# Performance work log

Hardware: AMD Instinct MI355X
Metric: run time of the kernel (lower is better)

Reference implementation:

```python
import jax, jax.numpy as jnp
import numpy as np

B, C, T = 8, 256, 2048
K = 10                     # n_neigh_seq
TEMPORAL_SCALE = 2048
SHORT_RATIO = 0.4
STITCH_GAP = 20


def setup_inputs() -> dict:
    key = jax.random.key(0)
    k1, k2, k3, k4 = jax.random.split(key, 4)
    x = jax.random.normal(k1, (B, C, T), dtype=jnp.float32)
    num_frms = jax.random.randint(k2, (B,), 0, 2048, dtype=jnp.int64 if jax.config.jax_enable_x64 else jnp.int32)
    W_conv = jax.random.normal(k3, (C, C, 3), dtype=jnp.float32) * 0.02  # Conv1d(out,in,k)
    b_conv = jnp.zeros((C,), dtype=jnp.float32)
    W_mlp = jax.random.normal(k4, (C, 2 * C), dtype=jnp.float32) * 0.02  # Linear(2C -> C)
    b_mlp = jnp.zeros((C,), dtype=jnp.float32)
    return {"x": x, "num_frms": num_frms, "W_conv": W_conv, "b_conv": b_conv,
            "W_mlp": W_mlp, "b_mlp": b_mlp}


def knn_neigh_idx(x, num_frms, k=K):
    """Vectorized translation of knn() + get_neigh_idx_semantic()."""
    b, c, t = x.shape
    ratio = TEMPORAL_SCALE / t
    half1 = k // 2
    half2 = k - half1
    # pairwise squared distances via ||xi||^2 + ||xj||^2 - 2 xi.xj (same math,
    # avoids the B*C*T*T intermediate the torch code materializes)
    sq = jnp.sum(x * x, axis=1)                           # [B,T]
    gram = jnp.einsum('bci,bcj->bij', x, x)               # [B,T,T]
    dif = sq[:, :, None] + sq[:, None, :] - 2.0 * gram    # [B,T,T]
    _, idx_org = jax.lax.top_k(-dif, k)                   # smallest-k -> [B,T,k]
    big = jnp.max(dif) + 1.0
    # per-batch short-video rewiring (original does a python loop over batch)
    cond = num_frms.astype(jnp.float32) <= SHORT_RATIO * TEMPORAL_SCALE   # [B]
    thr = (num_frms.astype(jnp.float32) + STITCH_GAP) / ratio             # [B]
    pos = jnp.arange(t)
    region = (pos[None, :, None] >= thr[:, None, None]) & \
             (pos[None, None, :] >= thr[:, None, None])                   # [B,T,T]
    dif_m = jnp.where(region, big, dif)
    # kill the already-chosen first half of neighbors, then re-topk the rest
    b_idx = jnp.arange(b)[:, None, None]
    r_idx = pos[None, :, None]
    dif_m = dif_m.at[b_idx, r_idx, idx_org[:, :, :half1]].set(big)
    _, idx2 = jax.lax.top_k(-dif_m, half2)                # [B,T,half2]
    tail = jnp.where(cond[:, None, None], idx2, idx_org[:, :, half1:])
    idx_new = jnp.concatenate([idx_org[:, :, :half1], tail], axis=-1)     # [B,T,k]
    shift = (jnp.arange(b) * t)[:, None, None]
    return (idx_new + shift).reshape(-1)                  # [B*T*k] flat node ids


def reference(x, num_frms, W_conv, b_conv, W_mlp, b_mlp):
    b, c, t = x.shape
    # tconv1: Conv1d k=3, s=1, p=1
    c_out = jax.lax.conv_general_dilated(
        x, W_conv, window_strides=(1,), padding=[(1, 1)],
        dimension_numbers=('NCH', 'OIH', 'NCH')) + b_conv[None, :, None]   # [B,C,T]
    # NeighConv on raw x (gcn_insert == 'par'), nfeat_mode='feat_ctr', agg='max'
    neigh = knn_neigh_idx(x, num_frms)                    # [B*T*K]
    feat = jnp.transpose(x, (0, 2, 1)).reshape(-1, c)     # [B*T, C]
    feat_neigh = feat[neigh].reshape(-1, K, c)            # [B*T, K, C]
    ctr = jnp.broadcast_to(feat[:, None, :], feat_neigh.shape)
    cat = jnp.concatenate([feat_neigh, ctr], axis=-1)     # [B*T, K, 2C]
    g = jnp.einsum('nkd,od->nko', cat, W_mlp) + b_mlp     # [B*T, K, C]
    g = jnp.max(g, axis=1)                                # max aggregation
    g_out = jnp.transpose(g.reshape(b, t, -1), (0, 2, 1)) # [B,C,T]
    out = jax.nn.relu(c_out + g_out)
    # MaxPool1d(kernel=2, stride=2)
    out = out.reshape(b, out.shape[1], t // 2, 2).max(axis=-1)
    return out
```

## Files before the change

### kernel.cpp

```cpp
#include <hip/hip_runtime.h>
#include <hip/hip_bf16.h>
#include <math.h>
#include <float.h>

#define NC 256
#define NT 2048

typedef __attribute__((ext_vector_type(4))) float f32x4;
typedef __attribute__((ext_vector_type(8))) short short8;
typedef __attribute__((ext_vector_type(8))) unsigned short ushort8;

#define SQ_OFF 0
#define A_OFF  131072
#define XL_OFF 8388608
#define E_OFF  16908288
#define NB_OFF 33685504

__device__ __forceinline__ int load_nf(const int* __restrict__ nf, int b) {
    bool is64 = (nf[1] == 0) & (nf[3] == 0) & (nf[5] == 0) & (nf[7] == 0);
    return is64 ? nf[2 * b] : nf[b];
}

__device__ __forceinline__ void split_bf16(float f, unsigned short& h, unsigned short& l) {
    __hip_bfloat16 hb = __float2bfloat16(f);
    float fh = __bfloat162float(hb);
    __hip_bfloat16 lb = __float2bfloat16(f - fh);
    h = *(unsigned short*)&hb;
    l = *(unsigned short*)&lb;
}

__device__ __forceinline__ float rl_f(float v, int srclane) {
    return __int_as_float(__builtin_amdgcn_readlane(__float_as_int(v), srclane));
}
__device__ __forceinline__ int rl_i(int v, int srclane) {
    return __builtin_amdgcn_readlane(v, srclane);
}
__device__ __forceinline__ float dpp_shr1_f(float v) {
    return __int_as_float(__builtin_amdgcn_update_dpp(0, __float_as_int(v), 0x111, 0xf, 0xf, false));
}
__device__ __forceinline__ int dpp_shr1_i(int v) {
    return __builtin_amdgcn_update_dpp(0, v, 0x111, 0xf, 0xf, false);
}

__global__ __launch_bounds__(256) void k_sqt(const float* __restrict__ x, double* __restrict__ sq,
                                             unsigned short* __restrict__ Xh8,
                                             unsigned short* __restrict__ Xl8,
                                             float* __restrict__ xT) {
    __shared__ double part[32][33];
    int b = blockIdx.y;
    int q0 = blockIdx.x * 32;
    int tid = threadIdx.x;
    int tq = tid & 7;
    int cg = tid >> 3;
    const float* xp = x + (size_t)b * NC * NT + q0 + tq * 4;
    double a0 = 0.0, a1 = 0.0, a2 = 0.0, a3 = 0.0;
    ushort8 hv[4], lw[4];
    float xv[4][8];
    #pragma unroll
    for (int i = 0; i < 8; ++i) {
        int c = cg * 8 + i;
        float4 f4 = *(const float4*)&xp[(size_t)c * NT];
        unsigned short h, l;
        split_bf16(f4.x, h, l); hv[0][i] = h; lw[0][i] = l; xv[0][i] = f4.x;
        a0 = fma((double)f4.x, (double)f4.x, a0);
        split_bf16(f4.y, h, l); hv[1][i] = h; lw[1][i] = l; xv[1][i] = f4.y;
        a1 = fma((double)f4.y, (double)f4.y, a1);
        split_bf16(f4.z, h, l); hv[2][i] = h; lw[2][i] = l; xv[2][i] = f4.z;
        a2 = fma((double)f4.z, (double)f4.z, a2);
        split_bf16(f4.w, h, l); hv[3][i] = h; lw[3][i] = l; xv[3][i] = f4.w;
        a3 = fma((double)f4.w, (double)f4.w, a3);
    }
    #pragma unroll
    for (int j = 0; j < 4; ++j) {
        int t = q0 + tq * 4 + j;
        size_t off = (((size_t)b * 32 + cg) * NT + t) * 8;
        *(ushort8*)(Xh8 + off) = hv[j];
        *(ushort8*)(Xl8 + off) = lw[j];
        float* xtr = &xT[((size_t)b * NT + t) * NC + cg * 8];
        *(float4*)xtr       = *(float4*)&xv[j][0];
        *(float4*)(xtr + 4) = *(float4*)&xv[j][4];
    }
    part[tq * 4 + 0][cg] = a0;
    part[tq * 4 + 1][cg] = a1;
    part[tq * 4 + 2][cg] = a2;
    part[tq * 4 + 3][cg] = a3;
    __syncthreads();
    if (tid < 32) {
        double s = 0.0;
        #pragma unroll
        for (int g = 0; g < 32; ++g) s += part[tid][g];
        sq[b * NT + q0 + tid] = s;
    }
}

__global__ __launch_bounds__(256) void k_wsplit(const float* __restrict__ Wc, const float* __restrict__ Wm,
                                                unsigned short* __restrict__ wsc) {
    int o = blockIdx.x;
    int tid = threadIdx.x;
    #pragma unroll
    for (int i = 0; i < 3; ++i) {
        int idx = i * 256 + tid;
        int c = idx / 3, kh = idx % 3;
        float w = Wc[(size_t)o * 768 + idx];
        if (kh == 1) w += Wm[(size_t)o * 512 + 256 + c];
        unsigned short h, l;
        split_bf16(w, h, l);
        wsc[(size_t)(kh * 256 + o) * 256 + c] = h;
        wsc[196608 + (size_t)(kh * 256 + o) * 256 + c] = l;
    }
    float wa = Wm[(size_t)o * 512 + tid];
    unsigned short h, l;
    split_bf16(wa, h, l);
    wsc[393216 + (size_t)o * 256 + tid] = h;
    wsc[458752 + (size_t)o * 256 + tid] = l;
}

#define XQH_S 264
#define DFB_S 130

__global__ __launch_bounds__(512, 8) void k_knn_a(const unsigned short* __restrict__ Xh8,
                                                  const unsigned short* __restrict__ Xl8,
                                                  const double* __restrict__ sq,
                                                  const int* __restrict__ nf,
                                                  unsigned short* __restrict__ cand,
                                                  unsigned short* __restrict__ cand2) {
    __shared__ __align__(16) unsigned short Qh[16 * XQH_S];
    __shared__ __align__(16) unsigned short Ql[16 * XQH_S];
    __shared__ __align__(16) float Df[2][16 * DFB_S];
    int q0 = blockIdx.x * 16;
    int b = blockIdx.y;
    int tid = threadIdx.x;
    int lane = tid & 63, wave = tid >> 6;
    const unsigned short* Xh8b = Xh8 + (size_t)b * 32 * NT * 8;
    const unsigned short* Xl8b = Xl8 + (size_t)b * 32 * NT * 8;
    const double* sqb = sq + b * NT;
    int n = load_nf(nf, b);
    int thr = n + 20;
    bool need2 = (n <= 819) && (q0 + 15 >= thr);
    float lv[2], lv2[2];
    int li[2], li2[2];
    #pragma unroll
    for (int rr = 0; rr < 2; ++rr) { lv[rr] = INFINITY; li[rr] = 0; lv2[rr] = INFINITY; li2[rr] = 0; }
    {
        int q = tid & 15, cgp = tid >> 4;
        size_t off = (((size_t)cgp) * NT + q0 + q) * 8;
        uint4 vh = *(const uint4*)(Xh8b + off);
        uint4 vl = *(const uint4*)(Xl8b + off);
        *(uint4*)&Qh[q * XQH_S + cgp * 8] = vh;
        *(uint4*)&Ql[q * XQH_S + cgp * 8] = vl;
    }
    int quad = lane >> 4, l15 = lane & 15;
    int qrow = l15;
    int n0 = wave * 16 + l15;
    float sqv[4];
    #pragma unroll
    for (int bb = 0; bb < 4; ++bb) sqv[bb] = (float)sqb[q0 + quad * 4 + bb];
    __syncthreads();
    int lane_elem = (quad * NT + n0) * 8;
#define LD_OCT(oct, koff, ph, pl) do { \
    int o_ = lane_elem + (oct) * 4 * NT * 8 + (koff) * 8; \
    ph = *(const short8*)(Xh8b + o_); \
    pl = *(const short8*)(Xl8b + o_); \
  } while (0)
    short8 hA[2], lA[2];
    LD_OCT(0, 0, hA[0], lA[0]);
    LD_OCT(1, 0, hA[1], lA[1]);
    for (int k0 = 0; k0 < NT; k0 += 128) {
        int knext = (k0 + 128 < NT) ? (k0 + 128) : k0;
        f32x4 acc0 = {0.f, 0.f, 0.f, 0.f};
        float sk0 = (float)sqb[k0 + n0];
        #pragma unroll
        for (int cc = 0; cc < 8; ++cc) {
            const int bi = cc & 1;
            short8 bh = hA[bi], bl = lA[bi];
            if (cc < 6) { LD_OCT(cc + 2, k0, hA[bi], lA[bi]); }
            else        { LD_OCT(cc - 6, knext, hA[bi], lA[bi]); }
            int cb = cc << 5;
            short8 ah = *(const short8*)&Qh[qrow * XQH_S + cb + quad * 8];
            short8 al = *(const short8*)&Ql[qrow * XQH_S + cb + quad * 8];
            acc0 = __builtin_amdgcn_mfma_f32_16x16x32_bf16(al, bh, acc0, 0, 0, 0);
            acc0 = __builtin_amdgcn_mfma_f32_16x16x32_bf16(ah, bl, acc0, 0, 0, 0);
            acc0 = __builtin_amdgcn_mfma_f32_16x16x32_bf16(ah, bh, acc0, 0, 0, 0);
        }
        int p = (k0 >> 7) & 1;
        float* DfP = Df[p];
        #pragma unroll
        for (int bb = 0; bb < 4; ++bb) {
            int mr = quad * 4 + bb;
            DfP[mr * DFB_S + n0] = sqv[bb] + sk0 - 2.f * acc0[bb];
        }
        __syncthreads();
        #pragma unroll
        for (int rr = 0; rr < 2; ++rr) {
            int row = wave * 2 + rr;
            #pragma unroll
            for (int g = 0; g < 2; ++g) {
                float d = DfP[row * DFB_S + g * 64 + lane];
                int kbase = k0 + g * 64;
                {
                    float thr16 = rl_f(lv[rr], 15);
                    unsigned long long mask = __ballot(d < thr16);
                    while (mask) {
                        int bit = __ffsll(mask) - 1;
                        mask &= mask - 1;
                        float vv = rl_f(d, bit);
                        int jj = kbase + bit;
                        unsigned long long le = __ballot(lv[rr] <= vv);
                        int pos = __popcll(le);
                        float pv = dpp_shr1_f(lv[rr]);
                        int pj = dpp_shr1_i(li[rr]);
                        if (lane < 16) {
                            if (lane == pos)      { lv[rr] = vv; li[rr] = jj; }
                            else if (lane > pos)  { lv[rr] = pv; li[rr] = pj; }
                        }
                        mask &= __ballot(d < rl_f(lv[rr], 15));
                    }
                }
                bool do2 = need2 && (kbase < thr);
                if (do2) {
                    unsigned long long vmask = __ballot((kbase + lane) < thr);
                    float thr24 = rl_f(lv2[rr], 23);
                    unsigned long long mask = __ballot(d < thr24) & vmask;
                    while (mask) {
                        int bit = __ffsll(mask) - 1;
                        mask &= mask - 1;
                        float vv = rl_f(d, bit);
                        int jj = kbase + bit;
                        unsigned long long le = __ballot(lv2[rr] <= vv);
                        int pos = __popcll(le);
                        float pv = dpp_shr1_f(lv2[rr]);
                        int pj = dpp_shr1_i(li2[rr]);
                        if (lane == 16) { pv = rl_f(lv2[rr], 15); pj = rl_i(li2[rr], 15); }
                        if (lane < 24) {
                            if (lane == pos)      { lv2[rr] = vv; li2[rr] = jj; }
                            else if (lane > pos)  { lv2[rr] = pv; li2[rr] = pj; }
                        }
                        mask &= __ballot(d < rl_f(lv2[rr], 23));
                    }
                }
            }
        }
    }
#undef LD_OCT
    if (lane < 16) {
        #pragma unroll
        for (int rr = 0; rr < 2; ++rr)
            cand[((size_t)b * NT + q0 + wave * 2 + rr) * 16 + lane] = (unsigned short)li[rr];
    }
    if (need2 && lane < 24) {
        #pragma unroll
        for (int rr = 0; rr < 2; ++rr) {
            unsigned short v = (lv2[rr] == INFINITY) ? 0xFFFFu : (unsigned short)li2[rr];
            cand2[((size_t)b * NT + q0 + wave * 2 + rr) * 24 + lane] = v;
        }
    }
}

__global__ __launch_bounds__(256) void k_rr(const float* __restrict__ xT, const double* __restrict__ sq,
                                            const int* __restrict__ nf,
                                            const unsigned short* __restrict__ cand,
                                            const unsigned short* __restrict__ cand2,
                                            int* __restrict__ nb) {
    int b = blockIdx.y;
    int wave = threadIdx.x >> 6, lane = threadIdx.x & 63;
    int t = blockIdx.x * 4 + wave;
    int n = load_nf(nf, b);
    int thr = n + 20;
    bool rr2row = (n <= 819) && (t >= thr);
    const float* qp = &xT[((size_t)b * NT + t) * NC];
    float4 q4 = *(const float4*)&qp[lane * 4];
    double sqt = sq[b * NT + t];
    int* nrow = &nb[((size_t)b * NT + t) * 10];
    const unsigned short* cr = &cand[((size_t)b * NT + t) * 16];
    double myd = 0.0; int myc = 0;
    for (int i = 0; i < 16; ++i) {
        int t2 = cr[i];
        float4 k4 = *(const float4*)&xT[((size_t)b * NT + t2) * NC + lane * 4];
        double s = fma((double)q4.w, (double)k4.w,
                   fma((double)q4.z, (double)k4.z,
                   fma((double)q4.y, (double)k4.y, (double)q4.x * (double)k4.x)));
        #pragma unroll
        for (int off = 32; off; off >>= 1) s += __shfl_xor(s, off);
        double d = sqt + sq[b * NT + t2] - 2.0 * s;
        if (lane == i) { myd = d; myc = t2; }
    }
    int rank = 0;
    for (int j = 0; j < 16; ++j) {
        double dj = __shfl(myd, j);
        int cj = __shfl(myc, j);
        if (lane < 16 && j != lane)
            rank += ((dj < myd) || (dj == myd && cj < myc)) ? 1 : 0;
    }
    if (lane < 16 && rank < 5) nrow[rank] = myc;
    bool w1hi = (lane < 16) && (rank >= 5) && (rank < 10);
    if (!rr2row) {
        if (w1hi) nrow[rank] = myc;
        return;
    }
    int f[5];
    #pragma unroll
    for (int s = 0; s < 5; ++s) {
        unsigned long long m = __ballot((lane < 16) && (rank == s));
        f[s] = __shfl(myc, __ffsll(m) - 1);
    }
    const unsigned short* cr2 = &cand2[((size_t)b * NT + t) * 24];
    double myd2 = DBL_MAX; int myc2 = 0x7FFFFFFF;
    for (int i = 0; i < 24; ++i) {
        int c16 = cr2[i];
        if (c16 == 0xFFFF) continue;
        int t2 = c16;
        float4 k4 = *(const float4*)&xT[((size_t)b * NT + t2) * NC + lane * 4];
        double s = fma((double)q4.w, (double)k4.w,
                   fma((double)q4.z, (double)k4.z,
                   fma((double)q4.y, (double)k4.y, (double)q4.x * (double)k4.x)));
        #pragma unroll
        for (int off = 32; off; off >>= 1) s += __shfl_xor(s, off);
        double d = sqt + sq[b * NT + t2] - 2.0 * s;
        if (lane == i) { myd2 = d; myc2 = t2; }
    }
    bool keep = (lane < 24) && (myc2 != 0x7FFFFFFF);
    #pragma unroll
    for (int s = 0; s < 5; ++s) keep = keep && (myc2 != f[s]);
    int rank2 = 0;
    for (int j = 0; j < 24; ++j) {
        double dj = __shfl(myd2, j);
        int cj = __shfl(myc2, j);
        bool kj = __shfl((int)keep, j);
        if (keep && kj && j != lane)
            rank2 += ((dj < myd2) || (dj == myd2 && cj < myc2)) ? 1 : 0;
    }
    int nK = __popcll(__ballot(keep)); if (nK > 5) nK = 5;
    if (keep && rank2 < 5) nrow[5 + rank2] = myc2;
    if (w1hi && (rank - 5) >= nK) nrow[rank] = myc;
}

#define XT_S 40

__global__ __launch_bounds__(256) void k_conv(const float* __restrict__ x, const unsigned short* __restrict__ wsc,
                                              const float* __restrict__ bc, const float* __restrict__ bm,
                                              float* __restrict__ E, float* __restrict__ A) {
    __shared__ __align__(16) unsigned short XTh[66 * XT_S], XTl[66 * XT_S];
    __shared__ __align__(16) unsigned short Wsh[3 * 64 * XT_S], Wsl[3 * 64 * XT_S];
    __shared__ __align__(16) unsigned short Wah[64 * XT_S], Wal[64 * XT_S];
    int tx = blockIdx.x * 64, oy = blockIdx.y * 64, b = blockIdx.z;
    int tid = threadIdx.x, lane = tid & 63, wave = tid >> 6;
    int quad = lane >> 4, l15 = lane & 15;
    f32x4 accE[4] = {}, accA[4] = {};
    for (int c0 = 0; c0 < 256; c0 += 32) {
        __syncthreads();
        #pragma unroll
        for (int i = 0; i < 8; ++i) {
            int c = wave * 8 + i;
            int t = lane;
            int g = tx - 1 + t;
            float v = (g >= 0 && g < NT) ? x[((size_t)b * NC + c0 + c) * NT + g] : 0.f;
            unsigned short h, l;
            split_bf16(v, h, l);
            XTh[t * XT_S + c] = h;
            XTl[t * XT_S + c] = l;
        }
        if (tid < 64) {
            int c = tid >> 1, t = 64 + (tid & 1);
            int g = tx - 1 + t;
            float v = (g < NT) ? x[((size_t)b * NC + c0 + c) * NT + g] : 0.f;
            unsigned short h, l;
            split_bf16(v, h, l);
            XTh[t * XT_S + c] = h;
            XTl[t * XT_S + c] = l;
        }
        #pragma unroll
        for (int i = 0; i < 3; ++i) {
            int gidx = i * 256 + tid;
            int kh = gidx >> 8;
            int o  = (gidx >> 2) & 63;
            int g4 = gidx & 3;
            uint4 vh = *(const uint4*)&wsc[(size_t)(kh * 256 + oy + o) * 256 + c0 + g4 * 8];
            *(uint4*)&Wsh[(kh * 64 + o) * XT_S + g4 * 8] = vh;
            uint4 vl = *(const uint4*)&wsc[196608 + (size_t)(kh * 256 + oy + o) * 256 + c0 + g4 * 8];
            *(uint4*)&Wsl[(kh * 64 + o) * XT_S + g4 * 8] = vl;
        }
        {
            int o = tid >> 2, g4 = tid & 3;
            uint4 vh = *(const uint4*)&wsc[393216 + (size_t)(oy + o) * 256 + c0 + g4 * 8];
            *(uint4*)&Wah[o * XT_S + g4 * 8] = vh;
            uint4 vl = *(const uint4*)&wsc[458752 + (size_t)(oy + o) * 256 + c0 + g4 * 8];
            *(uint4*)&Wal[o * XT_S + g4 * 8] = vl;
        }
        __syncthreads();
        int trow = wave * 16 + l15;
        short8 a_h[3], a_l[3];
        #pragma unroll
        for (int kh = 0; kh < 3; ++kh) {
            a_h[kh] = *(const short8*)&XTh[(trow + kh) * XT_S + quad * 8];
            a_l[kh] = *(const short8*)&XTl[(trow + kh) * XT_S + quad * 8];
        }
        #pragma unroll
        for (int ns = 0; ns < 4; ++ns) {
            int orow = ns * 16 + l15;
            short8 wa_h = *(const short8*)&Wah[orow * XT_S + quad * 8];
            short8 wa_l = *(const short8*)&Wal[orow * XT_S + quad * 8];
            accA[ns] = __builtin_amdgcn_mfma_f32_16x16x32_bf16(a_l[1], wa_h, accA[ns], 0, 0, 0);
            accA[ns] = __builtin_amdgcn_mfma_f32_16x16x32_bf16(a_h[1], wa_l, accA[ns], 0, 0, 0);
            accA[ns] = __builtin_amdgcn_mfma_f32_16x16x32_bf16(a_h[1], wa_h, accA[ns], 0, 0, 0);
            #pragma unroll
            for (int kh = 0; kh < 3; ++kh) {
                short8 w_h = *(const short8*)&Wsh[(kh * 64 + orow) * XT_S + quad * 8];
                short8 w_l = *(const short8*)&Wsl[(kh * 64 + orow) * XT_S + quad * 8];
                accE[ns] = __builtin_amdgcn_mfma_f32_16x16x32_bf16(a_l[kh], w_h, accE[ns], 0, 0, 0);
                accE[ns] = __builtin_amdgcn_mfma_f32_16x16x32_bf16(a_h[kh], w_l, accE[ns], 0, 0, 0);
                accE[ns] = __builtin_amdgcn_mfma_f32_16x16x32_bf16(a_h[kh], w_h, accE[ns], 0, 0, 0);
            }
        }
    }
    #pragma unroll
    for (int ns = 0; ns < 4; ++ns) {
        int o = oy + ns * 16 + l15;
        float bias = bc[o] + bm[o];
        #pragma unroll
        for (int r = 0; r < 4; ++r) {
            int t = tx + wave * 16 + quad * 4 + r;
            E[((size_t)b * NT + t) * 256 + o] = accE[ns][r] + bias;
            A[((size_t)b * NT + t) * 256 + o] = accA[ns][r];
        }
    }
}

__global__ __launch_bounds__(256) void k_epi(const float* __restrict__ A, const float* __restrict__ E,
                                             const int* __restrict__ nb, float* __restrict__ out) {
    __shared__ float buf[8 * 260];
    int p0 = blockIdx.x * 8;
    int b = blockIdx.y;
    int tid = threadIdx.x;
    int o4 = tid & 63;
    int pg = tid >> 6;
    #pragma unroll
    for (int pp2 = 0; pp2 < 2; ++pp2) {
        int pp = pg * 2 + pp2;
        int p = p0 + pp;
        float vm[4] = {0.f, 0.f, 0.f, 0.f};
        #pragma unroll
        for (int tt = 0; tt < 2; ++tt) {
            int t = p * 2 + tt;
            const int* nrow = &nb[((size_t)b * NT + t) * 10];
            float gm[4] = {-FLT_MAX, -FLT_MAX, -FLT_MAX, -FLT_MAX};
            #pragma unroll
            for (int k = 0; k < 10; ++k) {
                int t2 = nrow[k] & (NT - 1);
                float4 a = *(const float4*)&A[((size_t)b * NT + t2) * 256 + o4 * 4];
                gm[0] = fmaxf(gm[0], a.x); gm[1] = fmaxf(gm[1], a.y);
                gm[2] = fmaxf(gm[2], a.z); gm[3] = fmaxf(gm[3], a.w);
            }
            float4 e = *(const float4*)&E[((size_t)b * NT + t) * 256 + o4 * 4];
            vm[0] = fmaxf(vm[0], fmaxf(e.x + gm[0], 0.f));
            vm[1] = fmaxf(vm[1], fmaxf(e.y + gm[1], 0.f));
            vm[2] = fmaxf(vm[2], fmaxf(e.z + gm[2], 0.f));
            vm[3] = fmaxf(vm[3], fmaxf(e.w + gm[3], 0.f));
        }
        float4 v = {vm[0], vm[1], vm[2], vm[3]};
        *(float4*)&buf[pp * 260 + o4 * 4] = v;
    }
    __syncthreads();
    #pragma unroll
    for (int i = 0; i < 8; ++i) {
        int idx = tid + i * 256;
        int oo = idx >> 3, pp = idx & 7;
        out[((size_t)b * 256 + oo) * 1024 + p0 + pp] = buf[pp * 260 + oo];
    }
}

extern "C" void kernel_launch(void* const* d_in, const int* in_sizes, int n_in,
                              void* d_out, int out_size, void* d_ws, size_t ws_size,
                              hipStream_t stream) {
    const float* x  = (const float*)d_in[0];
    const int*   nf = (const int*)d_in[1];
    const float* Wc = (const float*)d_in[2];
    const float* bc = (const float*)d_in[3];
    const float* Wm = (const float*)d_in[4];
    const float* bm = (const float*)d_in[5];
    float* out = (float*)d_out;
    char* ws = (char*)d_ws;
    double* sq = (double*)(ws + SQ_OFF);
    float* A   = (float*)(ws + A_OFF);
    float* E   = (float*)(ws + E_OFF);
    int* nb    = (int*)(ws + NB_OFF);
    unsigned short* Xh8 = (unsigned short*)(ws + A_OFF);
    unsigned short* Xl8 = (unsigned short*)(ws + A_OFF + XL_OFF);
    float* xT = (float*)(ws + E_OFF);
    unsigned short* wsc   = (unsigned short*)d_out;
    unsigned short* cand  = (unsigned short*)d_out + (1 << 20);
    unsigned short* cand2 = (unsigned short*)d_out + (1 << 20) + (1 << 19);

    k_sqt<<<dim3(64, 8), dim3(256), 0, stream>>>(x, sq, Xh8, Xl8, xT);
    k_wsplit<<<dim3(256), dim3(256), 0, stream>>>(Wc, Wm, wsc);
    k_knn_a<<<dim3(128, 8), dim3(512), 0, stream>>>(Xh8, Xl8, sq, nf, cand, cand2);
    k_rr<<<dim3(512, 8), dim3(256), 0, stream>>>(xT, sq, nf, cand, cand2, nb);
    k_conv<<<dim3(32, 4, 8), dim3(256), 0, stream>>>(x, wsc, bc, bm, E, A);
    k_epi<<<dim3(128, 8), dim3(256), 0, stream>>>(A, E, nb, out);
}
```

Baseline: 424.8 us.

## Software-pipeline distance MFMA tile ahead of top-k selection in knn kernel

Restructures the distance/top-k loop so the MFMA tile for the next 128 columns is computed before the top-k insertion scan on the current tile. The next tile's distances go into the alternate Df buffer after the scan, with one barrier per iteration. The aim is to overlap MFMA latency and global loads with the ballot-driven selection work. In exchange it holds a second accumulator live, which raises register pressure.

```diff
diff --git a/kernel.cpp b/kernel.cpp
--- a/kernel.cpp
+++ b/kernel.cpp
@@ -162,34 +162,45 @@
     ph = *(const short8*)(Xh8b + o_); \
     pl = *(const short8*)(Xl8b + o_); \
   } while (0)
+#define TILE_MFMA(kt, kpf, accv) do { \
+    _Pragma("unroll") \
+    for (int cc = 0; cc < 8; ++cc) { \
+        const int bi = cc & 1; \
+        short8 bh = hA[bi], bl = lA[bi]; \
+        if (cc < 6) { LD_OCT(cc + 2, (kt), hA[bi], lA[bi]); } \
+        else        { LD_OCT(cc - 6, (kpf), hA[bi], lA[bi]); } \
+        int cb = cc << 5; \
+        short8 ah = *(const short8*)&Qh[qrow * XQH_S + cb + quad * 8]; \
+        short8 al = *(const short8*)&Ql[qrow * XQH_S + cb + quad * 8]; \
+        accv = __builtin_amdgcn_mfma_f32_16x16x32_bf16(al, bh, accv, 0, 0, 0); \
+        accv = __builtin_amdgcn_mfma_f32_16x16x32_bf16(ah, bl, accv, 0, 0, 0); \
+        accv = __builtin_amdgcn_mfma_f32_16x16x32_bf16(ah, bh, accv, 0, 0, 0); \
+    } \
+  } while (0)
     short8 hA[2], lA[2];
     LD_OCT(0, 0, hA[0], lA[0]);
     LD_OCT(1, 0, hA[1], lA[1]);
+    {
+        f32x4 acc0 = {0.f, 0.f, 0.f, 0.f};
+        float sk0 = (float)sqb[0 + n0];
+        TILE_MFMA(0, 128, acc0);
+        #pragma unroll
+        for (int bb = 0; bb < 4; ++bb)
+            Df[0][(quad * 4 + bb) * DFB_S + n0] = sqv[bb] + sk0 - 2.f * acc0[bb];
+    }
+    __syncthreads();
     for (int k0 = 0; k0 < NT; k0 += 128) {
-        int knext = (k0 + 128 < NT) ? (k0 + 128) : k0;
-        f32x4 acc0 = {0.f, 0.f, 0.f, 0.f};
-        float sk0 = (float)sqb[k0 + n0];
-        #pragma unroll
-        for (int cc = 0; cc < 8; ++cc) {
-            const int bi = cc & 1;
-            short8 bh = hA[bi], bl = lA[bi];
-            if (cc < 6) { LD_OCT(cc + 2, k0, hA[bi], lA[bi]); }
-            else        { LD_OCT(cc - 6, knext, hA[bi], lA[bi]); }
-            int cb = cc << 5;
-            short8 ah = *(const short8*)&Qh[qrow * XQH_S + cb + quad * 8];
-            short8 al = *(const short8*)&Ql[qrow * XQH_S + cb + quad * 8];
-            acc0 = __builtin_amdgcn_mfma_f32_16x16x32_bf16(al, bh, acc0, 0, 0, 0);
-            acc0 = __builtin_amdgcn_mfma_f32_16x16x32_bf16(ah, bl, acc0, 0, 0, 0);
-            acc0 = __builtin_amdgcn_mfma_f32_16x16x32_bf16(ah, bh, acc0, 0, 0, 0);
-        }
         int p = (k0 >> 7) & 1;
+        int kn = k0 + 128;
+        bool has_next = kn < NT;
+        f32x4 accN = {0.f, 0.f, 0.f, 0.f};
+        float skn = 0.f;
+        if (has_next) {
+            skn = (float)sqb[kn + n0];
+            int kpf = (kn + 128 < NT) ? kn + 128 : kn;
+            TILE_MFMA(kn, kpf, accN);
+        }
         float* DfP = Df[p];
-        #pragma unroll
-        for (int bb = 0; bb < 4; ++bb) {
-            int mr = quad * 4 + bb;
-            DfP[mr * DFB_S + n0] = sqv[bb] + sk0 - 2.f * acc0[bb];
-        }
-        __syncthreads();
         #pragma unroll
         for (int rr = 0; rr < 2; ++rr) {
             int row = wave * 2 + rr;
@@ -240,7 +251,15 @@
                 }
             }
         }
-    }
+        if (has_next) {
+            float* DfN = Df[p ^ 1];
+            #pragma unroll
+            for (int bb = 0; bb < 4; ++bb)
+                DfN[(quad * 4 + bb) * DFB_S + n0] = sqv[bb] + skn - 2.f * accN[bb];
+        }
+        __syncthreads();
+    }
+#undef TILE_MFMA
 #undef LD_OCT
     if (lane < 16) {
         #pragma unroll
```

After: 429.6 us. No clear change (+1.1%).
